# Kernel tuning notes

Measured on AMD Instinct MI355X. Metric: run time of the kernel, lower is better.

## Reference

```python
import jax, jax.numpy as jnp
import numpy as np

N, E, B = 50000, 500000, 500
NODE_IN, EDGE_IN = 64, 16
NODE_OUT, EDGE_OUT = 96, 64
FP_DIM, FP_EMBED = 2048, 128
HIDDEN = [512, 512]
OUT = 256
BN_EPS = 1e-5


def setup_inputs() -> dict:
    key = jax.random.key(0)
    ks = jax.random.split(key, 16)
    inp = {
        "node_feats": jax.random.normal(ks[0], (N, NODE_IN), jnp.float32),
        "edge_feats": jax.random.normal(ks[1], (E, EDGE_IN), jnp.float32),
        "fp_vector": jax.random.uniform(ks[2], (B, FP_DIM), jnp.float32),
        "src": jax.random.randint(ks[3], (E,), 0, N, dtype=jnp.int32),
        "dst": jax.random.randint(ks[4], (E,), 0, N, dtype=jnp.int32),
        "graph_ids": jnp.sort(jax.random.randint(ks[5], (N,), 0, B, dtype=jnp.int32)),
        # mpnn stand-in: single node projection
        "W_mpnn": jax.random.normal(ks[6], (NODE_IN, NODE_OUT), jnp.float32) / np.sqrt(NODE_IN),
        "b_mpnn": jnp.zeros((NODE_OUT,), jnp.float32),
        # project_edge_feats_module: linear edge projection
        "W_edge": jax.random.normal(ks[7], (EDGE_IN, EDGE_OUT), jnp.float32) / np.sqrt(EDGE_IN),
        "b_edge": jnp.zeros((EDGE_OUT,), jnp.float32),
        # FingerprintEncoder: Linear + BatchNorm1d (eval) + ReLU (+Dropout off)
        "W_fp": jax.random.normal(ks[8], (FP_DIM, FP_EMBED), jnp.float32) / np.sqrt(FP_DIM),
        "b_fp": jnp.zeros((FP_EMBED,), jnp.float32),
        "bn_gamma": jnp.ones((FP_EMBED,), jnp.float32),
        "bn_beta": jnp.zeros((FP_EMBED,), jnp.float32),
        "bn_mean": jnp.zeros((FP_EMBED,), jnp.float32),
        "bn_var": jnp.ones((FP_EMBED,), jnp.float32),
    }
    d_in = NODE_OUT + EDGE_OUT + FP_EMBED  # gnn_readout_dim + fp_embed_dim
    dims = [d_in] + HIDDEN + [OUT]
    for i in range(len(dims) - 1):
        inp[f"W_ffn{i}"] = jax.random.normal(ks[9 + i], (dims[i], dims[i + 1]), jnp.float32) / np.sqrt(dims[i])
        inp[f"b_ffn{i}"] = jnp.zeros((dims[i + 1],), jnp.float32)
    return inp


def reference(node_feats, edge_feats, fp_vector, src, dst, graph_ids,
              W_mpnn, b_mpnn, W_edge, b_edge,
              W_fp, b_fp, bn_gamma, bn_beta, bn_mean, bn_var,
              W_ffn0, b_ffn0, W_ffn1, b_ffn1, W_ffn2, b_ffn2):
    # mpnn node encodings [N, NODE_OUT]
    node_emb = node_feats @ W_mpnn + b_mpnn
    # projected edge embeddings [E, EDGE_OUT]
    edge_emb = edge_feats @ W_edge + b_edge
    # message: gather src node emb, concat edge emb -> [E, NODE_OUT+EDGE_OUT]
    msg = jnp.concatenate([node_emb[src], edge_emb], axis=1)
    # reduce: sum messages per destination node -> [N, NODE_OUT+EDGE_OUT]
    node_msg_sum = jax.ops.segment_sum(msg, dst, num_segments=N)
    # global_sum_pooling over nodes per graph -> [B, NODE_OUT+EDGE_OUT]
    mol = jax.ops.segment_sum(node_msg_sum, graph_ids, num_segments=B)
    mol = jax.nn.softmax(mol, axis=1)
    # fingerprint encoder (eval mode: BN uses running stats, dropout off)
    fp = fp_vector @ W_fp + b_fp
    fp = (fp - bn_mean) * jax.lax.rsqrt(bn_var + BN_EPS) * bn_gamma + bn_beta
    fp = jax.nn.relu(fp)
    # combined FFN (dropout off in eval)
    x = jnp.concatenate([mol, fp], axis=1)
    x = jax.nn.relu(x @ W_ffn0 + b_ffn0)
    x = jax.nn.relu(x @ W_ffn1 + b_ffn1)
    return x @ W_ffn2 + b_ffn2
```

## Files before the change

kernel.cpp:

```cpp
#include <hip/hip_runtime.h>
#include <math.h>

#define NODE_IN 64
#define NODE_OUT 96
#define EDGE_IN 16
#define EDGE_OUT 64
#define ACC_W 80
#define NB 500
#define FPD 2048
#define FPE 128
#define XDIM 288
#define BN_EPS 1e-5f
#define HB 1024
#define NBLKP 512

static __device__ __forceinline__ unsigned short f2bf(float f) {
    unsigned u = __float_as_uint(f);
    unsigned r = (u + 0x7fff + ((u >> 16) & 1)) >> 16;
    return (unsigned short)r;
}
static __device__ __forceinline__ float bflo(unsigned u) { return __uint_as_float(u << 16); }
static __device__ __forceinline__ float bfhi(unsigned u) { return __uint_as_float(u & 0xffff0000u); }

__global__ __launch_bounds__(1024) void hist_fp_kernel(
    const int* __restrict__ dst, const int* __restrict__ gids,
    int* __restrict__ gkey, int* __restrict__ pbhT, int nblk,
    const float* __restrict__ fpv, const float* __restrict__ Wf,
    float* __restrict__ pfp,
    const float* __restrict__ nf, unsigned short* __restrict__ nfb,
    int nfTot, int E)
{
    __shared__ int   h[NB];
    __shared__ float part[7][4][FPE];
    const int t = threadIdx.x;

    if (blockIdx.x >= nblk + NB) {
        const int b = blockIdx.x - nblk - NB;
        const size_t idx = ((size_t)b * 1024 + t) * 8;
        if (idx + 8 <= (size_t)nfTot) {
            const float4 a = *(const float4*)(nf + idx);
            const float4 c = *(const float4*)(nf + idx + 4);
            uint4 o;
            o.x = (unsigned)f2bf(a.x) | ((unsigned)f2bf(a.y) << 16);
            o.y = (unsigned)f2bf(a.z) | ((unsigned)f2bf(a.w) << 16);
            o.z = (unsigned)f2bf(c.x) | ((unsigned)f2bf(c.y) << 16);
            o.w = (unsigned)f2bf(c.z) | ((unsigned)f2bf(c.w) << 16);
            *(uint4*)(nfb + idx) = o;
        }
        return;
    }

    if (blockIdx.x >= nblk) {
        const int f   = blockIdx.x - nblk;
        const int rg  = f >> 2;
        const int ksl = f & 3;
        const int r0  = rg * 4;
        const int j   = t & 127;
        const int ks  = __builtin_amdgcn_readfirstlane(t >> 7);
        const int k0  = ksl * 512 + ks * 64;

        const float* __restrict__ xp0 = fpv + (size_t)(r0 + 0) * FPD + k0;
        const float* __restrict__ xp1 = fpv + (size_t)(r0 + 1) * FPD + k0;
        const float* __restrict__ xp2 = fpv + (size_t)(r0 + 2) * FPD + k0;
        const float* __restrict__ xp3 = fpv + (size_t)(r0 + 3) * FPD + k0;
        const float* __restrict__ wp  = Wf + (size_t)k0 * FPE + j;

        float a0 = 0.f, a1 = 0.f, a2 = 0.f, a3 = 0.f;
        for (int k = 0; k < 64; k += 8) {
            #pragma unroll
            for (int u = 0; u < 8; ++u) {
                const float w = wp[(size_t)(k + u) * FPE];
                a0 = fmaf(xp0[k + u], w, a0);
                a1 = fmaf(xp1[k + u], w, a1);
                a2 = fmaf(xp2[k + u], w, a2);
                a3 = fmaf(xp3[k + u], w, a3);
            }
        }
        if (ks > 0) {
            part[ks - 1][0][j] = a0; part[ks - 1][1][j] = a1;
            part[ks - 1][2][j] = a2; part[ks - 1][3][j] = a3;
        }
        __syncthreads();
        if (ks == 0) {
            #pragma unroll
            for (int qd = 0; qd < 7; ++qd) {
                a0 += part[qd][0][j]; a1 += part[qd][1][j];
                a2 += part[qd][2][j]; a3 += part[qd][3][j];
            }
            float* __restrict__ pp = pfp + ((size_t)ksl * NB + r0) * FPE + j;
            pp[0 * FPE] = a0; pp[1 * FPE] = a1;
            pp[2 * FPE] = a2; pp[3 * FPE] = a3;
        }
        return;
    }

    for (int i = t; i < NB; i += 1024) h[i] = 0;
    __syncthreads();
    const int e = blockIdx.x * HB + t;
    if (e < E) {
        const int g = gids[dst[e]];
        gkey[e] = g;
        atomicAdd(&h[g], 1);
    }
    __syncthreads();
    for (int i = t; i < NB; i += 1024)
        pbhT[(size_t)i * NBLKP + blockIdx.x] = h[i];
}

__global__ __launch_bounds__(512) void colscan_kernel(
    const int* __restrict__ pbhT, int* __restrict__ pcs,
    int* __restrict__ gsum, int nblk,
    const float* __restrict__ pfp, const float* __restrict__ bf,
    const float* __restrict__ gam, const float* __restrict__ bet,
    const float* __restrict__ mu, const float* __restrict__ var,
    float* __restrict__ xbuf)
{
    __shared__ int s[512];
    const int g = blockIdx.x;
    const int t = threadIdx.x;
    const int v0 = (t < nblk) ? pbhT[(size_t)g * NBLKP + t] : 0;
    s[t] = v0;
    __syncthreads();
    for (int d = 1; d < 512; d <<= 1) {
        const int v = (t >= d) ? s[t - d] : 0;
        __syncthreads();
        s[t] += v;
        __syncthreads();
    }
    if (t < nblk) pcs[(size_t)t * NB + g] = s[t] - v0;
    if (t == 511) gsum[g] = s[511];

    if (t < FPE) {
        const float a = (pfp[((size_t)0 * NB + g) * FPE + t] +
                         pfp[((size_t)1 * NB + g) * FPE + t]) +
                        (pfp[((size_t)2 * NB + g) * FPE + t] +
                         pfp[((size_t)3 * NB + g) * FPE + t]);
        const float sc = rsqrtf(var[t] + BN_EPS) * gam[t];
        const float sh = bet[t] - mu[t] * sc;
        xbuf[(size_t)g * XDIM + 160 + t] = fmaxf(fmaf(a + bf[t], sc, sh), 0.f);
    }
}

__global__ __launch_bounds__(1024) void scatter2_kernel(
    const int* __restrict__ gkey, const int* __restrict__ src,
    const int* __restrict__ pcs, const int* __restrict__ gsum,
    int2* __restrict__ sp, int* __restrict__ offs, int E)
{
    __shared__ int sc[512];
    __shared__ int offsL[NB];
    __shared__ int h[NB];
    __shared__ int basel[NB];
    const int t = threadIdx.x;

    int v0 = 0;
    if (t < 512) {
        v0 = (t < NB) ? gsum[t] : 0;
        sc[t] = v0;
    }
    __syncthreads();
    for (int d = 1; d < 512; d <<= 1) {
        int v = 0;
        if (t < 512 && t >= d) v = sc[t - d];
        __syncthreads();
        if (t < 512) sc[t] += v;
        __syncthreads();
    }
    if (t < NB) offsL[t] = sc[t] - v0;
    __syncthreads();

    for (int i = t; i < NB; i += 1024) {
        h[i] = 0;
        basel[i] = offsL[i] + pcs[(size_t)blockIdx.x * NB + i];
    }
    if (blockIdx.x == 0 && t < NB) offs[t] = offsL[t];
    __syncthreads();

    const int e = blockIdx.x * HB + t;
    if (e < E) {
        const int g = gkey[e];
        const int r = atomicAdd(&h[g], 1);
        sp[basel[g] + r] = make_int2(src[e], e);
    }
}

__global__ __launch_bounds__(1024) void graph_accum(
    const int2* __restrict__ sp,
    const unsigned short* __restrict__ nfb, const float* __restrict__ ef,
    const int* __restrict__ offs, const int* __restrict__ tot,
    const float* __restrict__ Wm, const float* __restrict__ bm,
    const float* __restrict__ We, const float* __restrict__ be,
    float* __restrict__ xbuf, int E)
{
    const int g = blockIdx.x;
    const int t = threadIdx.x;
    const int lane = t & 63;
    const int w = t >> 6;
    const int start = offs[g];
    const int cnt = tot[g];
    const int end = start + cnt;

    const uint4* __restrict__ nfb4 = (const uint4*)nfb;
    const float4* __restrict__ ef4 = (const float4*)ef;

    __shared__ float sacc[16][ACC_W];
    __shared__ float accRow[ACC_W];
    __shared__ float red[1024];

    const int eidx  = lane >> 3;
    const int chunk = lane & 7;
    const int eidx2 = lane >> 2;
    const int comp  = lane & 3;

    float nacc[8] = {};
    float eacc0 = 0.f, eacc1 = 0.f, eacc2 = 0.f, eacc3 = 0.f;

    for (int p0 = start + w * 64; p0 < end; p0 += 1024) {
        const int lim = min(64, end - p0);
        const int2 pr = sp[min(p0 + lane, E - 1)];
        const int sv = pr.x, ev = pr.y;

        #pragma unroll
        for (int r = 0; r < 2; ++r) {
            uint4 v[4];
            int ee[4];
            #pragma unroll
            for (int u = 0; u < 4; ++u) {
                ee[u] = (r * 4 + u) * 8 + eidx;
                const int s = __shfl(sv, ee[u]);
                v[u] = nfb4[(size_t)s * 8 + chunk];
            }
            #pragma unroll
            for (int u = 0; u < 4; ++u) {
                if (ee[u] < lim) {
                    nacc[0] += bflo(v[u].x); nacc[1] += bfhi(v[u].x);
                    nacc[2] += bflo(v[u].y); nacc[3] += bfhi(v[u].y);
                    nacc[4] += bflo(v[u].z); nacc[5] += bfhi(v[u].z);
                    nacc[6] += bflo(v[u].w); nacc[7] += bfhi(v[u].w);
                }
            }
        }

        {
            float4 v[4];
            int ee[4];
            #pragma unroll
            for (int u = 0; u < 4; ++u) {
                ee[u] = u * 16 + eidx2;
                const int eid = __shfl(ev, ee[u]);
                v[u] = ef4[(size_t)eid * 4 + comp];
            }
            #pragma unroll
            for (int u = 0; u < 4; ++u) {
                if (ee[u] < lim) {
                    eacc0 += v[u].x; eacc1 += v[u].y;
                    eacc2 += v[u].z; eacc3 += v[u].w;
                }
            }
        }
    }

    #pragma unroll
    for (int i = 0; i < 8; ++i) {
        nacc[i] += __shfl_xor(nacc[i], 8);
        nacc[i] += __shfl_xor(nacc[i], 16);
        nacc[i] += __shfl_xor(nacc[i], 32);
    }
    #pragma unroll
    for (int bit = 4; bit <= 32; bit <<= 1) {
        eacc0 += __shfl_xor(eacc0, bit);
        eacc1 += __shfl_xor(eacc1, bit);
        eacc2 += __shfl_xor(eacc2, bit);
        eacc3 += __shfl_xor(eacc3, bit);
    }
    if (lane < 8) {
        #pragma unroll
        for (int i = 0; i < 8; ++i)
            sacc[w][lane * 8 + i] = nacc[i];
    }
    if (lane < 4) {
        sacc[w][NODE_IN + lane * 4 + 0] = eacc0;
        sacc[w][NODE_IN + lane * 4 + 1] = eacc1;
        sacc[w][NODE_IN + lane * 4 + 2] = eacc2;
        sacc[w][NODE_IN + lane * 4 + 3] = eacc3;
    }
    __syncthreads();
    if (t < ACC_W) {
        float s = 0.f;
        #pragma unroll
        for (int w2 = 0; w2 < 16; ++w2) s += sacc[w2][t];
        accRow[t] = s;
    }
    __syncthreads();

    const float cntf = (float)cnt;
    float mr = 0.f;
    if (t < 96) {
        float m2 = 0.f;
        for (int k = 0; k < NODE_IN; ++k) m2 = fmaf(accRow[k], Wm[k * NODE_OUT + t], m2);
        mr = m2 + cntf * bm[t];
    } else if (t < 160) {
        const int j = t - 96;
        float m2 = 0.f;
        for (int k = 0; k < EDGE_IN; ++k) m2 = fmaf(accRow[NODE_IN + k], We[k * EDGE_OUT + j], m2);
        mr = m2 + cntf * be[j];
    }

    red[t] = (t < 160) ? mr : -1e30f;
    __syncthreads();
    for (int st = 512; st > 0; st >>= 1) {
        if (t < st) red[t] = fmaxf(red[t], red[t + st]);
        __syncthreads();
    }
    const float mx = red[0];
    __syncthreads();
    const float evx = (t < 160) ? expf(mr - mx) : 0.f;
    red[t] = evx;
    __syncthreads();
    for (int st = 512; st > 0; st >>= 1) {
        if (t < st) red[t] += red[t + st];
        __syncthreads();
    }
    if (t < 160) xbuf[(size_t)g * XDIM + t] = evx / red[0];
}

template<int NO>
__global__ __launch_bounds__(1024) void ffn_tile(
    const float* __restrict__ X, const float* __restrict__ W,
    const float* __restrict__ bias, float* __restrict__ Y,
    int Ni, int doRelu)
{
    __shared__ float part[7][4][128];
    const int t = threadIdx.x;
    const int col = t & 127;
    const int ks = __builtin_amdgcn_readfirstlane(t >> 7);
    const int r0 = blockIdx.x * 4;
    const int cg = blockIdx.y * 128 + col;
    const int kchunk = Ni >> 3;
    const int k0 = ks * kchunk;

    const float* __restrict__ xp0 = X + (size_t)(r0 + 0) * Ni + k0;
    const float* __restrict__ xp1 = X + (size_t)(r0 + 1) * Ni + k0;
    const float* __restrict__ xp2 = X + (size_t)(r0 + 2) * Ni + k0;
    const float* __restrict__ xp3 = X + (size_t)(r0 + 3) * Ni + k0;
    const float* __restrict__ wp  = W + (size_t)k0 * NO + cg;

    float a0 = 0.f, a1 = 0.f, a2 = 0.f, a3 = 0.f;
    for (int k = 0; k < kchunk; k += 4) {
        #pragma unroll
        for (int u = 0; u < 4; ++u) {
            const float w = wp[(size_t)(k + u) * NO];
            a0 = fmaf(xp0[k + u], w, a0);
            a1 = fmaf(xp1[k + u], w, a1);
            a2 = fmaf(xp2[k + u], w, a2);
            a3 = fmaf(xp3[k + u], w, a3);
        }
    }
    if (ks > 0) {
        part[ks - 1][0][col] = a0; part[ks - 1][1][col] = a1;
        part[ks - 1][2][col] = a2; part[ks - 1][3][col] = a3;
    }
    __syncthreads();
    if (ks == 0) {
        #pragma unroll
        for (int qd = 0; qd < 7; ++qd) {
            a0 += part[qd][0][col]; a1 += part[qd][1][col];
            a2 += part[qd][2][col]; a3 += part[qd][3][col];
        }
        const float bv = bias[cg];
        float o0 = a0 + bv, o1 = a1 + bv, o2 = a2 + bv, o3 = a3 + bv;
        if (doRelu) {
            o0 = fmaxf(o0, 0.f); o1 = fmaxf(o1, 0.f);
            o2 = fmaxf(o2, 0.f); o3 = fmaxf(o3, 0.f);
        }
        Y[(size_t)(r0 + 0) * NO + cg] = o0;
        Y[(size_t)(r0 + 1) * NO + cg] = o1;
        Y[(size_t)(r0 + 2) * NO + cg] = o2;
        Y[(size_t)(r0 + 3) * NO + cg] = o3;
    }
}

extern "C" void kernel_launch(void* const* d_in, const int* in_sizes, int n_in,
                              void* d_out, int out_size, void* d_ws, size_t ws_size,
                              hipStream_t stream)
{
    const float* node_feats = (const float*)d_in[0];
    const float* edge_feats = (const float*)d_in[1];
    const float* fpv        = (const float*)d_in[2];
    const int*   src        = (const int*)d_in[3];
    const int*   dst        = (const int*)d_in[4];
    const int*   gids       = (const int*)d_in[5];
    const float* Wm  = (const float*)d_in[6];
    const float* bm  = (const float*)d_in[7];
    const float* We  = (const float*)d_in[8];
    const float* be  = (const float*)d_in[9];
    const float* Wf  = (const float*)d_in[10];
    const float* bf  = (const float*)d_in[11];
    const float* gam = (const float*)d_in[12];
    const float* bet = (const float*)d_in[13];
    const float* mu  = (const float*)d_in[14];
    const float* var = (const float*)d_in[15];
    const float* W0  = (const float*)d_in[16];
    const float* b0  = (const float*)d_in[17];
    const float* W1  = (const float*)d_in[18];
    const float* b1  = (const float*)d_in[19];
    const float* W2  = (const float*)d_in[20];
    const float* b2  = (const float*)d_in[21];
    const int E = in_sizes[3];
    const int nfTot = in_sizes[0];
    const int nblk = (E + HB - 1) / HB;
    const int ncv = (nfTot / 8 + 1023) / 1024;

    float* xbuf  = (float*)d_ws;
    int2*  sp    = (int2*)(xbuf + (size_t)NB * XDIM);
    int*   gkey  = (int*)(sp + E);
    int*   pbhT  = gkey + E;
    int*   pcs   = pbhT + (size_t)NB * NBLKP;
    int*   gsum  = pcs + (size_t)nblk * NB;
    int*   offs  = gsum + NB;
    float* pfp   = (float*)(offs + NB);
    float* h1    = pfp + (size_t)4 * NB * FPE;
    float* h2    = h1 + (size_t)NB * 512;
    unsigned short* nfb = (unsigned short*)(h2 + (size_t)NB * 512);

    hipLaunchKernelGGL(hist_fp_kernel, dim3(nblk + NB + ncv), dim3(1024), 0, stream,
                       dst, gids, gkey, pbhT, nblk,
                       fpv, Wf, pfp, node_feats, nfb, nfTot, E);
    hipLaunchKernelGGL(colscan_kernel, dim3(NB), dim3(512), 0, stream,
                       pbhT, pcs, gsum, nblk,
                       pfp, bf, gam, bet, mu, var, xbuf);
    hipLaunchKernelGGL(scatter2_kernel, dim3(nblk), dim3(1024), 0, stream,
                       gkey, src, pcs, gsum, sp, offs, E);
    hipLaunchKernelGGL(graph_accum, dim3(NB), dim3(1024), 0, stream,
                       sp, nfb, edge_feats, offs, gsum,
                       Wm, bm, We, be, xbuf, E);
    hipLaunchKernelGGL((ffn_tile<512>), dim3(NB / 4, 4), dim3(1024), 0, stream,
                       xbuf, W0, b0, h1, XDIM, 1);
    hipLaunchKernelGGL((ffn_tile<512>), dim3(NB / 4, 4), dim3(1024), 0, stream,
                       h1, W1, b1, h2, 512, 1);
    hipLaunchKernelGGL((ffn_tile<256>), dim3(NB / 4, 2), dim3(1024), 0, stream,
                       h2, W2, b2, (float*)d_out, 512, 0);
}
```

Before: 92.69 us.

## Retile fingerprint and FFN GEMMs to 16 rows per block

Measured after the change: 242.5 us. 162% more time.

```diff
diff --git a/kernel.cpp b/kernel.cpp
--- a/kernel.cpp
+++ b/kernel.cpp
@@ -13,6 +13,7 @@
 #define BN_EPS 1e-5f
 #define HB 1024
 #define NBLKP 512
+#define NFPB 32
 
 static __device__ __forceinline__ unsigned short f2bf(float f) {
     unsigned u = __float_as_uint(f);
@@ -30,12 +31,11 @@
     const float* __restrict__ nf, unsigned short* __restrict__ nfb,
     int nfTot, int E)
 {
-    __shared__ int   h[NB];
-    __shared__ float part[7][4][FPE];
+    __shared__ int h[NB];
     const int t = threadIdx.x;
 
-    if (blockIdx.x >= nblk + NB) {
-        const int b = blockIdx.x - nblk - NB;
+    if (blockIdx.x >= nblk + NFPB) {
+        const int b = blockIdx.x - nblk - NFPB;
         const size_t idx = ((size_t)b * 1024 + t) * 8;
         if (idx + 8 <= (size_t)nfTot) {
             const float4 a = *(const float4*)(nf + idx);
@@ -51,46 +51,32 @@
     }
 
     if (blockIdx.x >= nblk) {
-        const int f   = blockIdx.x - nblk;
-        const int rg  = f >> 2;
-        const int ksl = f & 3;
-        const int r0  = rg * 4;
-        const int j   = t & 127;
-        const int ks  = __builtin_amdgcn_readfirstlane(t >> 7);
-        const int k0  = ksl * 512 + ks * 64;
-
-        const float* __restrict__ xp0 = fpv + (size_t)(r0 + 0) * FPD + k0;
-        const float* __restrict__ xp1 = fpv + (size_t)(r0 + 1) * FPD + k0;
-        const float* __restrict__ xp2 = fpv + (size_t)(r0 + 2) * FPD + k0;
-        const float* __restrict__ xp3 = fpv + (size_t)(r0 + 3) * FPD + k0;
-        const float* __restrict__ wp  = Wf + (size_t)k0 * FPE + j;
-
-        float a0 = 0.f, a1 = 0.f, a2 = 0.f, a3 = 0.f;
-        for (int k = 0; k < 64; k += 8) {
-            #pragma unroll
-            for (int u = 0; u < 8; ++u) {
+        const int rg = blockIdx.x - nblk;
+        const int r0 = rg * 16;
+        const int j  = t & 127;
+        const int ks = __builtin_amdgcn_readfirstlane(t >> 7);
+        const int k0 = ks * 256;
+
+        const float* xp[16];
+        #pragma unroll
+        for (int r = 0; r < 16; ++r)
+            xp[r] = fpv + (size_t)min(r0 + r, NB - 1) * FPD + k0;
+        const float* __restrict__ wp = Wf + (size_t)k0 * FPE + j;
+
+        float acc[16] = {};
+        for (int k = 0; k < 256; k += 4) {
+            #pragma unroll
+            for (int u = 0; u < 4; ++u) {
                 const float w = wp[(size_t)(k + u) * FPE];
-                a0 = fmaf(xp0[k + u], w, a0);
-                a1 = fmaf(xp1[k + u], w, a1);
-                a2 = fmaf(xp2[k + u], w, a2);
-                a3 = fmaf(xp3[k + u], w, a3);
+                #pragma unroll
+                for (int r = 0; r < 16; ++r)
+                    acc[r] = fmaf(xp[r][k + u], w, acc[r]);
             }
         }
-        if (ks > 0) {
-            part[ks - 1][0][j] = a0; part[ks - 1][1][j] = a1;
-            part[ks - 1][2][j] = a2; part[ks - 1][3][j] = a3;
-        }
-        __syncthreads();
-        if (ks == 0) {
-            #pragma unroll
-            for (int qd = 0; qd < 7; ++qd) {
-                a0 += part[qd][0][j]; a1 += part[qd][1][j];
-                a2 += part[qd][2][j]; a3 += part[qd][3][j];
-            }
-            float* __restrict__ pp = pfp + ((size_t)ksl * NB + r0) * FPE + j;
-            pp[0 * FPE] = a0; pp[1 * FPE] = a1;
-            pp[2 * FPE] = a2; pp[3 * FPE] = a3;
-        }
+        float* __restrict__ pp = pfp + (size_t)ks * NB * FPE;
+        #pragma unroll
+        for (int r = 0; r < 16; ++r)
+            if (r0 + r < NB) pp[(size_t)(r0 + r) * FPE + j] = acc[r];
         return;
     }
 
@@ -131,10 +117,10 @@
     if (t == 511) gsum[g] = s[511];
 
     if (t < FPE) {
-        const float a = (pfp[((size_t)0 * NB + g) * FPE + t] +
-                         pfp[((size_t)1 * NB + g) * FPE + t]) +
-                        (pfp[((size_t)2 * NB + g) * FPE + t] +
-                         pfp[((size_t)3 * NB + g) * FPE + t]);
+        float a = 0.f;
+        #pragma unroll
+        for (int sl = 0; sl < 8; ++sl)
+            a += pfp[((size_t)sl * NB + g) * FPE + t];
         const float sc = rsqrtf(var[t] + BN_EPS) * gam[t];
         const float sh = bet[t] - mu[t] * sc;
         xbuf[(size_t)g * XDIM + 160 + t] = fmaxf(fmaf(a + bf[t], sc, sh), 0.f);
@@ -324,58 +310,53 @@
 }
 
 template<int NO>
-__global__ __launch_bounds__(1024) void ffn_tile(
+__global__ __launch_bounds__(512) void ffn_tile16(
     const float* __restrict__ X, const float* __restrict__ W,
     const float* __restrict__ bias, float* __restrict__ Y,
     int Ni, int doRelu)
 {
-    __shared__ float part[7][4][128];
+    __shared__ float part[3][16][128];
     const int t = threadIdx.x;
     const int col = t & 127;
     const int ks = __builtin_amdgcn_readfirstlane(t >> 7);
-    const int r0 = blockIdx.x * 4;
+    const int r0 = blockIdx.x * 16;
     const int cg = blockIdx.y * 128 + col;
-    const int kchunk = Ni >> 3;
+    const int kchunk = Ni >> 2;
     const int k0 = ks * kchunk;
 
-    const float* __restrict__ xp0 = X + (size_t)(r0 + 0) * Ni + k0;
-    const float* __restrict__ xp1 = X + (size_t)(r0 + 1) * Ni + k0;
-    const float* __restrict__ xp2 = X + (size_t)(r0 + 2) * Ni + k0;
-    const float* __restrict__ xp3 = X + (size_t)(r0 + 3) * Ni + k0;
-    const float* __restrict__ wp  = W + (size_t)k0 * NO + cg;
-
-    float a0 = 0.f, a1 = 0.f, a2 = 0.f, a3 = 0.f;
+    const float* xp[16];
+    #pragma unroll
+    for (int r = 0; r < 16; ++r)
+        xp[r] = X + (size_t)min(r0 + r, NB - 1) * Ni + k0;
+    const float* __restrict__ wp = W + (size_t)k0 * NO + cg;
+
+    float acc[16] = {};
     for (int k = 0; k < kchunk; k += 4) {
         #pragma unroll
         for (int u = 0; u < 4; ++u) {
             const float w = wp[(size_t)(k + u) * NO];
-            a0 = fmaf(xp0[k + u], w, a0);
-            a1 = fmaf(xp1[k + u], w, a1);
-            a2 = fmaf(xp2[k + u], w, a2);
-            a3 = fmaf(xp3[k + u], w, a3);
+            #pragma unroll
+            for (int r = 0; r < 16; ++r)
+                acc[r] = fmaf(xp[r][k + u], w, acc[r]);
         }
     }
     if (ks > 0) {
-        part[ks - 1][0][col] = a0; part[ks - 1][1][col] = a1;
-        part[ks - 1][2][col] = a2; part[ks - 1][3][col] = a3;
+        #pragma unroll
+        for (int r = 0; r < 16; ++r) part[ks - 1][r][col] = acc[r];
     }
     __syncthreads();
     if (ks == 0) {
         #pragma unroll
-        for (int qd = 0; qd < 7; ++qd) {
-            a0 += part[qd][0][col]; a1 += part[qd][1][col];
-            a2 += part[qd][2][col]; a3 += part[qd][3][col];
-        }
+        for (int q = 0; q < 3; ++q)
+            #pragma unroll
+            for (int r = 0; r < 16; ++r) acc[r] += part[q][r][col];
         const float bv = bias[cg];
-        float o0 = a0 + bv, o1 = a1 + bv, o2 = a2 + bv, o3 = a3 + bv;
-        if (doRelu) {
-            o0 = fmaxf(o0, 0.f); o1 = fmaxf(o1, 0.f);
-            o2 = fmaxf(o2, 0.f); o3 = fmaxf(o3, 0.f);
-        }
-        Y[(size_t)(r0 + 0) * NO + cg] = o0;
-        Y[(size_t)(r0 + 1) * NO + cg] = o1;
-        Y[(size_t)(r0 + 2) * NO + cg] = o2;
-        Y[(size_t)(r0 + 3) * NO + cg] = o3;
+        #pragma unroll
+        for (int r = 0; r < 16; ++r) {
+            float o = acc[r] + bv;
+            if (doRelu) o = fmaxf(o, 0.f);
+            if (r0 + r < NB) Y[(size_t)(r0 + r) * NO + cg] = o;
+        }
     }
 }
 
@@ -418,11 +399,11 @@
     int*   gsum  = pcs + (size_t)nblk * NB;
     int*   offs  = gsum + NB;
     float* pfp   = (float*)(offs + NB);
-    float* h1    = pfp + (size_t)4 * NB * FPE;
+    float* h1    = pfp + (size_t)8 * NB * FPE;
     float* h2    = h1 + (size_t)NB * 512;
     unsigned short* nfb = (unsigned short*)(h2 + (size_t)NB * 512);
 
-    hipLaunchKernelGGL(hist_fp_kernel, dim3(nblk + NB + ncv), dim3(1024), 0, stream,
+    hipLaunchKernelGGL(hist_fp_kernel, dim3(nblk + NFPB + ncv), dim3(1024), 0, stream,
                        dst, gids, gkey, pbhT, nblk,
                        fpv, Wf, pfp, node_feats, nfb, nfTot, E);
     hipLaunchKernelGGL(colscan_kernel, dim3(NB), dim3(512), 0, stream,
@@ -433,10 +414,10 @@
     hipLaunchKernelGGL(graph_accum, dim3(NB), dim3(1024), 0, stream,
                        sp, nfb, edge_feats, offs, gsum,
                        Wm, bm, We, be, xbuf, E);
-    hipLaunchKernelGGL((ffn_tile<512>), dim3(NB / 4, 4), dim3(1024), 0, stream,
+    hipLaunchKernelGGL((ffn_tile16<512>), dim3(32, 4), dim3(512), 0, stream,
                        xbuf, W0, b0, h1, XDIM, 1);
-    hipLaunchKernelGGL((ffn_tile<512>), dim3(NB / 4, 4), dim3(1024), 0, stream,
+    hipLaunchKernelGGL((ffn_tile16<512>), dim3(32, 4), dim3(512), 0, stream,
                        h1, W1, b1, h2, 512, 1);
-    hipLaunchKernelGGL((ffn_tile<256>), dim3(NB / 4, 2), dim3(1024), 0, stream,
+    hipLaunchKernelGGL((ffn_tile16<256>), dim3(32, 2), dim3(512), 0, stream,
                        h2, W2, b2, (float*)d_out, 512, 0);
 }
```
